# Kernel tuning notes

Hardware: AMD Instinct MI355X
Metric: run time of the kernel (lower is better)

## Reference

```python
import jax, jax.numpy as jnp
import numpy as np

B, S, BERT_H = 8, 512, 432
NL, HD = 12, 64
H = NL * HD  # 768
NEG = -1e12

def _lin(k, i, o):
    return jax.random.normal(k, (i, o), jnp.float32) * 0.02

def setup_inputs():
    key = jax.random.key(0)
    ks = jax.random.split(key, 12)
    return {
        "bert_hidden": jax.random.normal(ks[0], (B, S, BERT_H), jnp.float32),
        "attention_mask": jnp.ones((B, S), jnp.float32),
        "dense_w": _lin(ks[1], BERT_H, H), "dense_b": jnp.zeros((H,)),
        "sat_qw": _lin(ks[2], H, H), "sat_qb": jnp.zeros((H,)),
        "sat_kw": _lin(ks[3], H, H), "sat_kb": jnp.zeros((H,)),
        "sat_vw": _lin(ks[4], H, H), "sat_vb": jnp.zeros((H,)),
        "sat_ow": _lin(ks[5], H, H), "sat_ob": jnp.zeros((H,)),
        "rel_qw": _lin(ks[6], H, H), "rel_qb": jnp.zeros((H,)),
        "rel_kw": _lin(ks[7], H, H), "rel_kb": jnp.zeros((H,)),
        "rel_vw": _lin(ks[8], H, H), "rel_vb": jnp.zeros((H,)),
        "rel_ow": _lin(ks[9], H, H), "rel_ob": jnp.zeros((H,)),
        "lns_w": jnp.ones((H,)), "lns_b": jnp.zeros((H,)),
        "lnr_w": jnp.ones((H,)), "lnr_b": jnp.zeros((H,)),
        "head_w": _lin(ks[10], H, 2 * HD), "head_b": jnp.zeros((2 * HD,)),
        "tail_w": _lin(ks[11], 2 * HD, 2 * NL), "tail_b": jnp.zeros((2 * NL,)),
    }

def _layernorm(x, w, b, eps=1e-12):
    u = x.mean(-1, keepdims=True)
    s = ((x - u) ** 2).mean(-1, keepdims=True)
    return w * (x - u) / jnp.sqrt(s + eps) + b

def _mha(q_in, k_in, v_in, wq, bq, wk, bk, wv, bv, wo, bo):
    # q_in: [N, Lq, H]; k_in/v_in: [N, Lk, H]; dropout is identity (eval)
    N, Lq, _ = q_in.shape
    Lk = k_in.shape[1]
    qh = (q_in @ wq + bq).reshape(N, Lq, NL, HD)
    kh = (k_in @ wk + bk).reshape(N, Lk, NL, HD)
    vh = (v_in @ wv + bv).reshape(N, Lk, NL, HD)
    scores = jnp.einsum('nqhd,nkhd->nhqk', qh, kh) / np.float32(np.sqrt(HD))
    probs = jax.nn.softmax(scores, axis=-1)
    ctx = jnp.einsum('nhqk,nkhd->nqhd', probs, vh).reshape(N, Lq, NL * HD)
    return ctx @ wo + bo + q_in

def _shift_back(x):
    # faithful torch cycle_shift(forward=False): circular roll left by 1
    return jnp.roll(x, -1, axis=1)

def _shift_fwd(x):
    # faithful to the torch sequential in-place loop in cycle_shift(forward=True):
    # out[0] = x[-1]; out[1:] = x[0] (each copy reads the already-overwritten slot)
    b, s, h = x.shape
    return jnp.concatenate([x[:, -1:, :], jnp.broadcast_to(x[:, :1, :], (b, s - 1, h))], axis=1)

def reference(bert_hidden, attention_mask, dense_w, dense_b,
              sat_qw, sat_qb, sat_kw, sat_kb, sat_vw, sat_vb, sat_ow, sat_ob,
              rel_qw, rel_qb, rel_kw, rel_kb, rel_vw, rel_vb, rel_ow, rel_ob,
              lns_w, lns_b, lnr_w, lnr_b, head_w, head_b, tail_w, tail_b):
    hidden0 = bert_hidden @ dense_w + dense_b  # [B,S,H]
    cs = hidden0
    center = cs.mean(axis=1)  # [B,H], avg_pool2d over seq dim
    for _ in range(2):
        before = _shift_back(cs)
        after = _shift_fwd(cs)
        center_exp = jnp.broadcast_to(center[:, None, :], cs.shape)
        concats = jnp.stack([before, cs, after, hidden0, center_exp], axis=2)  # [B,S,5,H]
        concats = concats.reshape(B * S, 5, H)
        q = cs.reshape(B * S, 1, H)
        sat = _mha(q, concats, concats, sat_qw, sat_qb, sat_kw, sat_kb, sat_vw, sat_vb, sat_ow, sat_ob)
        cs = _layernorm(jax.nn.relu(sat), lns_w, lns_b).reshape(B, S, H)
        cc = jnp.concatenate([center[:, None, :], cs], axis=1)  # [B,S+1,H]
        rel = _mha(center[:, None, :], cc, cc, rel_qw, rel_qb, rel_kw, rel_kb, rel_vw, rel_vb, rel_ow, rel_ob)
        center = _layernorm(jax.nn.relu(rel), lnr_w, lnr_b)[:, 0, :]
    outputs = cs @ head_w + head_b  # [B,S,2*HD]
    qw, kw = outputs[..., ::2], outputs[..., 1::2]  # [B,S,HD]
    pos = jnp.arange(S, dtype=jnp.float32)
    inv = jnp.power(10000.0, -2.0 * jnp.arange(HD // 2, dtype=jnp.float32) / HD)
    ang = pos[:, None] * inv[None, :]  # [S,HD//2]
    pe = jnp.stack([jnp.sin(ang), jnp.cos(ang)], axis=-1).reshape(S, HD)
    cos_pos = jnp.repeat(pe[:, 1::2], 2, axis=-1)  # [S,HD]
    sin_pos = jnp.repeat(pe[:, ::2], 2, axis=-1)
    def rot(x):
        x2 = jnp.stack([-x[..., 1::2], x[..., ::2]], axis=-1).reshape(x.shape)
        return x * cos_pos + x2 * sin_pos
    qw, kw = rot(qw), rot(kw)
    logits = jnp.einsum('bmd,bnd->bmn', qw, kw) / np.float32(np.sqrt(HD))  # [B,S,S]
    bias = jnp.einsum('bnh->bhn', outputs @ tail_w + tail_b) / 2.0  # [B,2*NL,S]
    logits = logits[:, None, :, :] + bias[:, ::2, None, :] + bias[:, 1::2, :, None]  # [B,NL,S,S]
    m1 = attention_mask[:, None, :, None]
    logits = logits * m1 + NEG * (1.0 - m1)
    m2 = attention_mask[:, None, None, :]
    logits = logits * m2 + NEG * (1.0 - m2)
    tril = jnp.tril(jnp.ones((S, S), logits.dtype), k=-1)
    return logits - tril * 1e12
```

## Files before the change

### kernel.cpp

```cpp
#include <hip/hip_runtime.h>
#include <cstdint>
#include <cstddef>

#define HH 768
#define SS 512
#define NBATCH 8
#define NLH 12
#define HDIM 64
#define BSROWS 4096
static constexpr float NEGV = -1000000000000.0f;

typedef unsigned short ushort_t;
typedef __attribute__((ext_vector_type(4))) float fx4;
typedef __attribute__((ext_vector_type(8))) short sx8;

__device__ __forceinline__ ushort_t f2bf(float f) {
  uint32_t u = __float_as_uint(f);
  uint32_t r = (u + 0x7FFFu + ((u >> 16) & 1u)) >> 16;
  return (ushort_t)r;
}
__device__ __forceinline__ float bf2f(ushort_t h) {
  return __uint_as_float(((uint32_t)h) << 16);
}
__device__ __forceinline__ float2 ldbf2(const ushort_t* p) {
  uint32_t u = *(const uint32_t*)p;
  return make_float2(__uint_as_float(u << 16), __uint_as_float(u & 0xffff0000u));
}

__device__ __forceinline__ void async_copy16(void* lds, const void* g) {
  __builtin_amdgcn_global_load_lds(
      (const __attribute__((address_space(1))) void*)g,
      (__attribute__((address_space(3))) void*)lds, 16, 0, 0);
}

__device__ __forceinline__ void gemm_core(
    char* arena, int bid, int nwg, int nx,
    const ushort_t* __restrict__ A, int lda,
    const ushort_t* __restrict__ B, int ldb,
    const float* __restrict__ bias,
    const ushort_t* __restrict__ resb,
    ushort_t* __restrict__ Cb, int ldo,
    ushort_t* __restrict__ Cb2, int ldo2, int nsplit, int K,
    float* __restrict__ colmean)
{
  ushort_t* As = (ushort_t*)arena;
  ushort_t* Bs = (ushort_t*)(arena + 16384);
  const int tid = threadIdx.x;
  const int q = nwg >> 3;
  const int xcd = bid & 7, sidx = bid >> 3;
  const int swz = xcd * q + sidx;
  const int bm = (swz / nx) * 128;
  const int bn = (swz % nx) * 128;
  const int l = tid & 63;
  const int w = tid >> 6;
  const int wr = w >> 1, wc = w & 1;
  const int r8 = tid >> 3;
  const int sl = tid & 7;

  fx4 acc[4][4];
#pragma unroll
  for (int m = 0; m < 4; ++m)
#pragma unroll
    for (int n = 0; n < 4; ++n) acc[m][n] = (fx4)0.f;

  for (int k0 = 0; k0 < K; k0 += 64) {
#pragma unroll
    for (int i = 0; i < 4; ++i) {
      int row = i * 32 + r8;
      int srcs = sl ^ (row & 7);
      async_copy16((char*)As + i * 4096 + tid * 16,
                   A + (size_t)(bm + row) * lda + k0 + srcs * 8);
    }
#pragma unroll
    for (int i = 0; i < 4; ++i) {
      int row = i * 32 + r8;
      int srcs = sl ^ (row & 7);
      async_copy16((char*)Bs + i * 4096 + tid * 16,
                   B + (size_t)(bn + row) * ldb + k0 + srcs * 8);
    }
    __syncthreads();
#pragma unroll
    for (int kk = 0; kk < 2; ++kk) {
      sx8 av[4], bv[4];
      const int so = (l >> 4) + kk * 4;
#pragma unroll
      for (int m = 0; m < 4; ++m) {
        int r = wr * 64 + m * 16 + (l & 15);
        av[m] = *(const sx8*)((const char*)As + r * 128 + ((so ^ (r & 7)) * 16));
      }
#pragma unroll
      for (int n = 0; n < 4; ++n) {
        int r = wc * 64 + n * 16 + (l & 15);
        bv[n] = *(const sx8*)((const char*)Bs + r * 128 + ((so ^ (r & 7)) * 16));
      }
#pragma unroll
      for (int m = 0; m < 4; ++m)
#pragma unroll
        for (int n = 0; n < 4; ++n)
          acc[m][n] = __builtin_amdgcn_mfma_f32_16x16x32_bf16(av[m], bv[n], acc[m][n], 0, 0, 0);
    }
    __syncthreads();
  }

  const bool second = (bn >= nsplit);
  ushort_t* dst = second ? Cb2 : Cb;
  const int ld = second ? ldo2 : ldo;
  const int csub = second ? nsplit : 0;
  const int cr0 = bm + wr * 64 + (l >> 4) * 4;
  const int cc0 = bn + wc * 64 + (l & 15);
#pragma unroll
  for (int m = 0; m < 4; ++m) {
#pragma unroll
    for (int n = 0; n < 4; ++n) {
      int col = cc0 + n * 16;
      float bcol = bias[col];
#pragma unroll
      for (int j = 0; j < 4; ++j) {
        int row = cr0 + m * 16 + j;
        size_t off = (size_t)row * ld + (col - csub);
        float v = acc[m][n][j] + bcol;
        if (resb) v += bf2f(resb[off]);
        dst[off] = f2bf(v);
      }
    }
  }

  if (colmean) {
    float* scr = (float*)arena;
    const int cid = wr * 4 + (l >> 4);
#pragma unroll
    for (int n = 0; n < 4; ++n) {
      int colL = wc * 64 + n * 16 + (l & 15);
      float t = 16.0f * bias[bn + colL];
#pragma unroll
      for (int m = 0; m < 4; ++m)
#pragma unroll
        for (int j = 0; j < 4; ++j) t += acc[m][n][j];
      scr[cid * 128 + colL] = t;
    }
    __syncthreads();
    if (tid < 128) {
      float scol = 0.f;
#pragma unroll
      for (int c = 0; c < 8; ++c) scol += scr[c * 128 + tid];
      atomicAdd(&colmean[(bm >> 9) * HH + bn + tid], scol * (1.0f / 512.0f));
    }
  }
}

struct SmallJob { const float* W; const float* bias; const float* res; float* C; };
struct SmallJobs { SmallJob j[5]; };

__device__ __forceinline__ void skinny_core(
    char* arena, int colblk,
    const float* __restrict__ A, const float* __restrict__ W,
    const float* __restrict__ bias, const float* __restrict__ res, float* __restrict__ C)
{
  float* As = (float*)arena;
  float* part = (float*)(arena + 24576);
  const int tid = threadIdx.x;
#pragma unroll
  for (int i = 0; i < 6; ++i) {
    int idx = tid * 4 + i * 1024;
    *(float4*)&As[idx] = *(const float4*)(A + idx);
  }
  __syncthreads();
  const int c = tid & 31;
  const int col = (colblk << 5) + c;
  const int ks = tid >> 5;
  const float* Wp = W + (size_t)(ks * 96) * HH + col;
  float acc[8] = {};
#pragma unroll 8
  for (int k = 0; k < 96; ++k) {
    float wv = Wp[(size_t)k * HH];
    const float* ap = &As[ks * 96 + k];
#pragma unroll
    for (int m = 0; m < 8; ++m)
      acc[m] = fmaf(ap[m * HH], wv, acc[m]);
  }
#pragma unroll
  for (int m = 0; m < 8; ++m)
    part[ks * 256 + m * 32 + c] = acc[m];
  __syncthreads();
  const int m = tid >> 5;
  const int c2 = tid & 31;
  float s = 0.f;
#pragma unroll
  for (int k = 0; k < 8; ++k) s += part[k * 256 + m * 32 + c2];
  const int outcol = (colblk << 5) + c2;
  float v = s + bias[outcol];
  if (res) v += res[(size_t)m * HH + outcol];
  C[(size_t)m * HH + outcol] = v;
}

__global__ __launch_bounds__(256) void gemm_bf16(
    const ushort_t* __restrict__ A, int lda,
    const ushort_t* __restrict__ B, int ldb,
    const float* __restrict__ bias,
    const ushort_t* __restrict__ resb,
    ushort_t* __restrict__ Cb, int ldo,
    ushort_t* __restrict__ Cb2, int ldo2, int nsplit, int K, int nx,
    float* __restrict__ colmean)
{
  __shared__ char arena[32768];
  gemm_core(arena, blockIdx.x, gridDim.x, nx, A, lda, B, ldb, bias, resb,
            Cb, ldo, Cb2, ldo2, nsplit, K, colmean);
}

__global__ __launch_bounds__(256) void qkv_center(
    const ushort_t* __restrict__ A, const ushort_t* __restrict__ B,
    const float* __restrict__ bias, ushort_t* __restrict__ Cb,
    SmallJobs jobs, const float* __restrict__ center)
{
  __shared__ char arena[32768];
  if (blockIdx.x < 576) {
    gemm_core(arena, blockIdx.x, 576, 18, A, HH, B, HH, bias, nullptr,
              Cb, 2304, nullptr, 0, 1 << 30, HH, nullptr);
  } else {
    int vb = blockIdx.x - 576;
    SmallJob jb = jobs.j[vb / 24];
    skinny_core(arena, vb % 24, center, jb.W, jb.bias, jb.res, jb.C);
  }
}

__global__ __launch_bounds__(256) void gemm_skinny(
    const float* __restrict__ A, SmallJobs jobs)
{
  __shared__ char arena[32768];
  SmallJob jb = jobs.j[blockIdx.y];
  skinny_core(arena, blockIdx.x, A, jb.W, jb.bias, jb.res, jb.C);
}

struct SmallJobs2 { SmallJob j[2]; };
__global__ __launch_bounds__(256) void skinny_ln(
    const float* __restrict__ relo, const float* __restrict__ lw, const float* __restrict__ lb,
    SmallJobs2 jobs)
{
  __shared__ float As[8 * HH];
  __shared__ float part[8 * 8 * 32];
  const int tid = threadIdx.x;
  const SmallJob job = jobs.j[blockIdx.y];
#pragma unroll
  for (int i = 0; i < 6; ++i) {
    int idx = tid * 4 + i * 1024;
    *(float4*)&As[idx] = *(const float4*)(relo + idx);
  }
  __syncthreads();
  {
    const int row = tid >> 5, lc = tid & 31;
    float s = 0.f, sq = 0.f;
#pragma unroll
    for (int e = 0; e < 24; ++e) {
      float x = fmaxf(As[row * HH + lc * 24 + e], 0.f);
      s += x; sq += x * x;
    }
#pragma unroll
    for (int d = 1; d < 32; d <<= 1) { s += __shfl_xor(s, d); sq += __shfl_xor(sq, d); }
    float mean = s * (1.0f / HH);
    float var = sq * (1.0f / HH) - mean * mean;
    float rstd = rsqrtf(var + 1e-12f);
#pragma unroll
    for (int e = 0; e < 24; ++e) {
      int cc = lc * 24 + e;
      float x = fmaxf(As[row * HH + cc], 0.f);
      As[row * HH + cc] = lw[cc] * (x - mean) * rstd + lb[cc];
    }
  }
  __syncthreads();
  const int c = tid & 31;
  const int col = (blockIdx.x << 5) + c;
  const int ks = tid >> 5;
  const float* Wp = job.W + (size_t)(ks * 96) * HH + col;
  float acc[8] = {};
#pragma unroll 8
  for (int k = 0; k < 96; ++k) {
    float wv = Wp[(size_t)k * HH];
    const float* ap = &As[ks * 96 + k];
#pragma unroll
    for (int m = 0; m < 8; ++m)
      acc[m] = fmaf(ap[m * HH], wv, acc[m]);
  }
#pragma unroll
  for (int m = 0; m < 8; ++m)
    part[ks * 256 + m * 32 + c] = acc[m];
  __syncthreads();
  const int m = tid >> 5;
  const int c2 = tid & 31;
  float s2 = 0.f;
#pragma unroll
  for (int k = 0; k < 8; ++k) s2 += part[k * 256 + m * 32 + c2];
  const int outcol = (blockIdx.x << 5) + c2;
  job.C[(size_t)m * HH + outcol] = s2 + job.bias[outcol];
}

__global__ __launch_bounds__(256) void rel_attn(
    const float* __restrict__ Qr, const float* __restrict__ Krc, const ushort_t* __restrict__ Kr,
    const float* __restrict__ Vrc, const ushort_t* __restrict__ Vr, int ldkv,
    float* __restrict__ ctx)
{
  int b = blockIdx.x, h = blockIdx.y;
  __shared__ float qs[64];
  __shared__ float sc[513];
  __shared__ float part[4][64];
  __shared__ float redm[4], redsum[4];
  int t = threadIdx.x, lane = t & 63, wave = t >> 6;
  if (t < 64) qs[t] = Qr[b * HH + h * HDIM + t];
  __syncthreads();
  for (int j = t; j < 513; j += 256) {
    float acc = 0.f;
    if (j == 0) {
      const float* kp = Krc + b * HH + h * HDIM;
#pragma unroll
      for (int d = 0; d < HDIM; ++d) acc = fmaf(qs[d], kp[d], acc);
    } else {
      const sx8* kv = (const sx8*)(Kr + (size_t)(b * SS + j - 1) * ldkv + h * HDIM);
#pragma unroll
      for (int dq = 0; dq < 8; ++dq) {
        sx8 v = kv[dq];
#pragma unroll
        for (int e = 0; e < 8; ++e)
          acc = fmaf(qs[dq * 8 + e], bf2f((ushort_t)v[e]), acc);
      }
    }
    sc[j] = acc * 0.125f;
  }
  __syncthreads();
  float m = -1e30f;
  for (int j = t; j < 513; j += 256) m = fmaxf(m, sc[j]);
#pragma unroll
  for (int d = 1; d < 64; d <<= 1) m = fmaxf(m, __shfl_xor(m, d));
  if (lane == 0) redm[wave] = m;
  __syncthreads();
  m = fmaxf(fmaxf(redm[0], redm[1]), fmaxf(redm[2], redm[3]));
  float lsum = 0.f;
  for (int j = t; j < 513; j += 256) { float e = __expf(sc[j] - m); sc[j] = e; lsum += e; }
#pragma unroll
  for (int d = 1; d < 64; d <<= 1) lsum += __shfl_xor(lsum, d);
  if (lane == 0) redsum[wave] = lsum;
  __syncthreads();
  float total = redsum[0] + redsum[1] + redsum[2] + redsum[3];
  float accv = 0.f;
#pragma unroll 8
  for (int j = wave; j < 513; j += 4) {
    float vv = (j == 0) ? Vrc[b * HH + h * HDIM + lane]
                        : bf2f(Vr[(size_t)(b * SS + j - 1) * ldkv + h * HDIM + lane]);
    accv = fmaf(sc[j], vv, accv);
  }
  part[wave][lane] = accv;
  __syncthreads();
  if (wave == 0) {
    float r = (part[0][lane] + part[1][lane] + part[2][lane] + part[3][lane]) / total;
    ctx[b * HH + h * HDIM + lane] = r;
  }
}

__global__ __launch_bounds__(256) void head_fused(
    const ushort_t* __restrict__ Araw,
    const float* __restrict__ lnw, const float* __restrict__ lnb,
    const ushort_t* __restrict__ B,
    const float* __restrict__ head_b,
    const float* __restrict__ tail_w,
    const float* __restrict__ tail_b,
    float* __restrict__ qw, float* __restrict__ kw,
    float* __restrict__ bias2)
{
  __shared__ ushort_t As[16 * 64];
  __shared__ ushort_t Bs[128 * 64];
  __shared__ float tile[16][130];
  __shared__ float invt[32];
  __shared__ float2 rst[16];
  const int tid = threadIdx.x;
  const int bm = blockIdx.x * 16;
  const int l = tid & 63;
  const int w = tid >> 6;
  const int r8 = tid >> 3;
  const int sl = tid & 7;

  if (tid < 32) invt[tid] = powf(10000.0f, -(float)tid / 32.0f);

  {
    int row = tid >> 4, part = tid & 15;
    const ushort_t* rp = Araw + (size_t)(bm + row) * HH + part * 48;
    float s = 0.f, sq = 0.f;
#pragma unroll
    for (int c = 0; c < 6; ++c) {
      sx8 v = *(const sx8*)(rp + c * 8);
#pragma unroll
      for (int e = 0; e < 8; ++e) {
        float x = fmaxf(bf2f((ushort_t)v[e]), 0.f);
        s += x; sq += x * x;
      }
    }
#pragma unroll
    for (int d = 1; d < 16; d <<= 1) { s += __shfl_xor(s, d); sq += __shfl_xor(sq, d); }
    if (part == 0) {
      float mean = s * (1.0f / HH);
      float var = sq * (1.0f / HH) - mean * mean;
      rst[row] = make_float2(mean, rsqrtf(var + 1e-12f));
    }
  }
  __syncthreads();

  fx4 acc[2];
  acc[0] = (fx4)0.f; acc[1] = (fx4)0.f;

  for (int k0 = 0; k0 < HH; k0 += 64) {
#pragma unroll
    for (int i = 0; i < 4; ++i) {
      int row = i * 32 + r8;
      int srcs = sl ^ (row & 7);
      async_copy16((char*)Bs + i * 4096 + tid * 16,
                   B + (size_t)row * HH + k0 + srcs * 8);
    }
    if (tid < 128) {
      int row = tid >> 3;
      int slot = sl ^ (row & 7);
      int gk = k0 + slot * 8;
      sx8 v = *(const sx8*)(Araw + (size_t)(bm + row) * HH + gk);
      float4 w0 = *(const float4*)(lnw + gk);
      float4 w1 = *(const float4*)(lnw + gk + 4);
      float4 b0 = *(const float4*)(lnb + gk);
      float4 b1 = *(const float4*)(lnb + gk + 4);
      float wv[8] = {w0.x, w0.y, w0.z, w0.w, w1.x, w1.y, w1.z, w1.w};
      float bv[8] = {b0.x, b0.y, b0.z, b0.w, b1.x, b1.y, b1.z, b1.w};
      float2 mr = rst[row];
      sx8 ov;
#pragma unroll
      for (int e = 0; e < 8; ++e) {
        float x = fmaxf(bf2f((ushort_t)v[e]), 0.f);
        ov[e] = (short)f2bf(fmaf((x - mr.x) * mr.y, wv[e], bv[e]));
      }
      *(sx8*)((char*)As + row * 128 + sl * 16) = ov;
    }
    __syncthreads();
#pragma unroll
    for (int kk = 0; kk < 2; ++kk) {
      const int so = (l >> 4) + kk * 4;
      int ra = l & 15;
      sx8 av = *(const sx8*)((const char*)As + ra * 128 + ((so ^ (ra & 7)) * 16));
#pragma unroll
      for (int n = 0; n < 2; ++n) {
        int r = w * 32 + n * 16 + (l & 15);
        sx8 bv = *(const sx8*)((const char*)Bs + r * 128 + ((so ^ (r & 7)) * 16));
        acc[n] = __builtin_amdgcn_mfma_f32_16x16x32_bf16(av, bv, acc[n], 0, 0, 0);
      }
    }
    __syncthreads();
  }

  {
    const int rr0 = (l >> 4) * 4;
#pragma unroll
    for (int n = 0; n < 2; ++n) {
      int col = w * 32 + n * 16 + (l & 15);
      float bcol = head_b[col];
#pragma unroll
      for (int j = 0; j < 4; ++j)
        tile[rr0 + j][col] = acc[n][j] + bcol;
    }
  }
  __syncthreads();

#pragma unroll
  for (int it = 0; it < 2; ++it) {
    int t = tid + it * 256;
    int r = t >> 5, i = t & 31;
    int s = (bm + r) & 511;
    float ang = (float)s * invt[i];
    float sn = sinf(ang), cn = cosf(ang);
    float q0 = tile[r][4 * i + 0], k0 = tile[r][4 * i + 1];
    float q1 = tile[r][4 * i + 2], k1 = tile[r][4 * i + 3];
    float* qp = qw + (size_t)(bm + r) * 64 + i * 2;
    float* kp = kw + (size_t)(bm + r) * 64 + i * 2;
    qp[0] = q0 * cn - q1 * sn; qp[1] = q1 * cn + q0 * sn;
    kp[0] = k0 * cn - k1 * sn; kp[1] = k1 * cn + k0 * sn;
  }
  for (int t = tid; t < 16 * 24; t += 256) {
    int r = t / 24, c = t % 24;
    float acc2 = tail_b[c];
#pragma unroll 16
    for (int k = 0; k < 128; ++k) acc2 = fmaf(tile[r][k], tail_w[k * 24 + c], acc2);
    bias2[(size_t)(bm + r) * 24 + c] = acc2 * 0.5f;
  }
}

struct TJob { const float* src; ushort_t* dst; int K, N, Kpad, rowOff; };
struct PrepArgs {
  TJob j[8];
  const float* bert; ushort_t* bert_bf;
  const float* rkb; const float* rvb; const float* sqb; const float* skb; const float* svb;
  float* b_merged;
  float* center;
};
__global__ __launch_bounds__(256) void prep_all(PrepArgs pa)
{
  if (blockIdx.z < 8) {
    TJob jb = pa.j[blockIdx.z];
    int k0 = blockIdx.x * 32, n0 = blockIdx.y * 32;
    if (k0 >= jb.Kpad || n0 >= jb.N) return;
    __shared__ float t[32][33];
    int tx = threadIdx.x & 31, ty = threadIdx.x >> 5;
#pragma unroll
    for (int i = 0; i < 4; ++i) {
      int k = k0 + ty + i * 8;
      float v = 0.f;
      if (k < jb.K && n0 + tx < jb.N) v = jb.src[(size_t)k * jb.N + n0 + tx];
      t[ty + i * 8][tx] = v;
    }
    __syncthreads();
#pragma unroll
    for (int i = 0; i < 4; ++i) {
      int n = n0 + ty + i * 8;
      int k = k0 + tx;
      if (n < jb.N && k < jb.Kpad)
        jb.dst[(size_t)(jb.rowOff + n) * jb.Kpad + k] = f2bf(t[tx][ty + i * 8]);
    }
  } else {
    const int NB = BSROWS * 448;
    const int total = NB + 3840 + NBATCH * HH;
    int start = (blockIdx.y * 24 + blockIdx.x) * 256 + threadIdx.x;
    for (int i = start; i < total; i += 24 * 24 * 256) {
      if (i < NB) {
        int r = i / 448, c = i % 448;
        pa.bert_bf[i] = (c < 432) ? f2bf(pa.bert[(size_t)r * 432 + c]) : (ushort_t)0;
      } else if (i < NB + 3840) {
        int c = i - NB;
        float v;
        if (c < 768) v = pa.rkb[c];
        else if (c < 1536) v = pa.rvb[c - 768];
        else if (c < 2304) v = pa.sqb[c - 1536];
        else if (c < 3072) v = pa.skb[c - 2304];
        else v = pa.svb[c - 3072];
        pa.b_merged[c] = v;
      } else {
        pa.center[i - NB - 3840] = 0.f;
      }
    }
  }
}

__global__ __launch_bounds__(256) void sat_attn(
    const ushort_t* __restrict__ Qc, const ushort_t* __restrict__ Kc,
    const ushort_t* __restrict__ Vc, int ldq,
    const ushort_t* __restrict__ Kh0, const ushort_t* __restrict__ Vh0, int ldh,
    const float* __restrict__ Kcen, const float* __restrict__ Vcen,
    ushort_t* __restrict__ ctxb)
{
  int i = blockIdx.x;
  int b = i >> 9, s = i & 511;
  int lane = threadIdx.x & 63;
  int wave = threadIdx.x >> 6;
  size_t rb = (size_t)(b * SS + ((s + 1) & 511));
  size_t rs = (size_t)i;
  size_t ra = (size_t)(b * SS + (s == 0 ? (SS - 1) : 0));
  size_t rc = (size_t)b * HH;
  const int half = lane >> 5;
  const int d0 = (lane & 31) * 2;
#pragma unroll
  for (int it = 0; it < 2; ++it) {
    int p = wave + 4 * it;
    if (p >= 6) break;
    int off = (2 * p + half) * HDIM + d0;
    float2 q  = ldbf2(Qc + rs * ldq + off);
    float2 kb = ldbf2(Kc + rb * ldq + off);
    float2 ks = ldbf2(Kc + rs * ldq + off);
    float2 ka = ldbf2(Kc + ra * ldq + off);
    float2 kh = ldbf2(Kh0 + rs * ldh + off);
    float2 kc = *(const float2*)(Kcen + rc + off);
    float s0 = q.x * kb.x + q.y * kb.y;
    float s1 = q.x * ks.x + q.y * ks.y;
    float s2 = q.x * ka.x + q.y * ka.y;
    float s3 = q.x * kh.x + q.y * kh.y;
    float s4 = q.x * kc.x + q.y * kc.y;
#pragma unroll
    for (int d = 1; d < 32; d <<= 1) {
      s0 += __shfl_xor(s0, d); s1 += __shfl_xor(s1, d); s2 += __shfl_xor(s2, d);
      s3 += __shfl_xor(s3, d); s4 += __shfl_xor(s4, d);
    }
    const float sc = 0.125f;
    s0 *= sc; s1 *= sc; s2 *= sc; s3 *= sc; s4 *= sc;
    float mx = fmaxf(fmaxf(fmaxf(s0, s1), fmaxf(s2, s3)), s4);
    float e0 = __expf(s0 - mx), e1 = __expf(s1 - mx), e2 = __expf(s2 - mx);
    float e3 = __expf(s3 - mx), e4 = __expf(s4 - mx);
    float inv = 1.f / (e0 + e1 + e2 + e3 + e4);
    float2 vb = ldbf2(Vc + rb * ldq + off);
    float2 vs = ldbf2(Vc + rs * ldq + off);
    float2 va = ldbf2(Vc + ra * ldq + off);
    float2 vh = ldbf2(Vh0 + rs * ldh + off);
    float2 vc = *(const float2*)(Vcen + rc + off);
    float vx = e0 * vb.x + e1 * vs.x + e2 * va.x + e3 * vh.x + e4 * vc.x;
    float vy = e0 * vb.y + e1 * vs.y + e2 * va.y + e3 * vh.y + e4 * vc.y;
    uint32_t o = (uint32_t)f2bf(vx * inv) | ((uint32_t)f2bf(vy * inv) << 16);
    *(uint32_t*)(ctxb + rs * HH + off) = o;
  }
}

__global__ __launch_bounds__(256) void relu_ln_bf(
    const ushort_t* __restrict__ x, const float* __restrict__ w, const float* __restrict__ b,
    ushort_t* __restrict__ ybf)
{
  int row = blockIdx.x;
  const ushort_t* xr = x + (size_t)row * HH;
  float v[3];
  float sum = 0.f, sumsq = 0.f;
#pragma unroll
  for (int j = 0; j < 3; ++j) {
    float t = bf2f(xr[threadIdx.x + j * 256]);
    t = fmaxf(t, 0.f);
    v[j] = t;
    sum += t; sumsq += t * t;
  }
#pragma unroll
  for (int d = 1; d < 64; d <<= 1) { sum += __shfl_xor(sum, d); sumsq += __shfl_xor(sumsq, d); }
  __shared__ float ws_[4], wsq_[4];
  int wave = threadIdx.x >> 6, lane = threadIdx.x & 63;
  if (lane == 0) { ws_[wave] = sum; wsq_[wave] = sumsq; }
  __syncthreads();
  sum = ws_[0] + ws_[1] + ws_[2] + ws_[3];
  sumsq = wsq_[0] + wsq_[1] + wsq_[2] + wsq_[3];
  float mean = sum * (1.0f / HH);
  float var = sumsq * (1.0f / HH) - mean * mean;
  float rstd = rsqrtf(var + 1e-12f);
#pragma unroll
  for (int j = 0; j < 3; ++j) {
    int cidx = threadIdx.x + j * 256;
    float o = w[cidx] * (v[j] - mean) * rstd + b[cidx];
    ybf[(size_t)row * HH + cidx] = f2bf(o);
  }
}

__global__ __launch_bounds__(256) void final_kernel(
    const float* __restrict__ qw, const float* __restrict__ kw,
    const float* __restrict__ bias2, const float* __restrict__ mask,
    float* __restrict__ out)
{
  int b = blockIdx.z;
  int mt = blockIdx.y * 32;
  int nt = blockIdx.x * 32;
  __shared__ float qs[32][68];
  __shared__ float ks[32][68];
  int t = threadIdx.x;
  {
    int idx = t * 8;
    int r = idx >> 6, c = idx & 63;
    const float* sq = qw + (size_t)(b * SS + mt + r) * 64 + c;
    const float* sk = kw + (size_t)(b * SS + nt + r) * 64 + c;
    *(float4*)&qs[r][c]     = *(const float4*)(sq);
    *(float4*)&qs[r][c + 4] = *(const float4*)(sq + 4);
    *(float4*)&ks[r][c]     = *(const float4*)(sk);
    *(float4*)&ks[r][c + 4] = *(const float4*)(sk + 4);
  }
  __syncthreads();
  int m = t >> 3;
  int n0 = (t & 7) * 4;
  float d0 = 0.f, d1 = 0.f, d2 = 0.f, d3 = 0.f;
#pragma unroll
  for (int d = 0; d < 64; d += 4) {
    float4 qv = *(const float4*)&qs[m][d];
    float4 k0 = *(const float4*)&ks[n0 + 0][d];
    float4 k1 = *(const float4*)&ks[n0 + 1][d];
    float4 k2 = *(const float4*)&ks[n0 + 2][d];
    float4 k3 = *(const float4*)&ks[n0 + 3][d];
    d0 += qv.x * k0.x + qv.y * k0.y + qv.z * k0.z + qv.w * k0.w;
    d1 += qv.x * k1.x + qv.y * k1.y + qv.z * k1.z + qv.w * k1.w;
    d2 += qv.x * k2.x + qv.y * k2.y + qv.z * k2.z + qv.w * k2.w;
    d3 += qv.x * k3.x + qv.y * k3.y + qv.z * k3.z + qv.w * k3.w;
  }
  int gm = mt + m;
  int gn = nt + n0;
  d0 *= 0.125f; d1 *= 0.125f; d2 *= 0.125f; d3 *= 0.125f;
  float mm = mask[b * SS + gm];
  float mn0 = mask[b * SS + gn + 0];
  float mn1 = mask[b * SS + gn + 1];
  float mn2 = mask[b * SS + gn + 2];
  float mn3 = mask[b * SS + gn + 3];
  const float* bmp  = bias2 + (size_t)(b * SS + gm) * 24;
  const float* bnp0 = bias2 + (size_t)(b * SS + gn + 0) * 24;
  const float* bnp1 = bias2 + (size_t)(b * SS + gn + 1) * 24;
  const float* bnp2 = bias2 + (size_t)(b * SS + gn + 2) * 24;
  const float* bnp3 = bias2 + (size_t)(b * SS + gn + 3) * 24;
#pragma unroll
  for (int h = 0; h < NLH; ++h) {
    float tb = bmp[2 * h + 1];
    float v0 = d0 + bnp0[2 * h] + tb;
    float v1 = d1 + bnp1[2 * h] + tb;
    float v2 = d2 + bnp2[2 * h] + tb;
    float v3 = d3 + bnp3[2 * h] + tb;
    v0 = v0 * mm + NEGV * (1.f - mm); v1 = v1 * mm + NEGV * (1.f - mm);
    v2 = v2 * mm + NEGV * (1.f - mm); v3 = v3 * mm + NEGV * (1.f - mm);
    v0 = v0 * mn0 + NEGV * (1.f - mn0); v1 = v1 * mn1 + NEGV * (1.f - mn1);
    v2 = v2 * mn2 + NEGV * (1.f - mn2); v3 = v3 * mn3 + NEGV * (1.f - mn3);
    if (gm > gn + 0) v0 -= 1000000000000.0f;
    if (gm > gn + 1) v1 -= 1000000000000.0f;
    if (gm > gn + 2) v2 -= 1000000000000.0f;
    if (gm > gn + 3) v3 -= 1000000000000.0f;
    float4 o = make_float4(v0, v1, v2, v3);
    *(float4*)(out + ((((size_t)(b * NLH + h)) * SS + gm) * SS + gn)) = o;
  }
}

extern "C" void kernel_launch(void* const* d_in, const int* in_sizes, int n_in,
                              void* d_out, int out_size, void* d_ws, size_t ws_size,
                              hipStream_t stream)
{
  const float* bert    = (const float*)d_in[0];
  const float* amask   = (const float*)d_in[1];
  const float* dense_w = (const float*)d_in[2];
  const float* dense_b = (const float*)d_in[3];
  const float* sat_qw  = (const float*)d_in[4];
  const float* sat_qb  = (const float*)d_in[5];
  const float* sat_kw  = (const float*)d_in[6];
  const float* sat_kb  = (const float*)d_in[7];
  const float* sat_vw  = (const float*)d_in[8];
  const float* sat_vb  = (const float*)d_in[9];
  const float* sat_ow  = (const float*)d_in[10];
  const float* sat_ob  = (const float*)d_in[11];
  const float* rel_qw  = (const float*)d_in[12];
  const float* rel_qb  = (const float*)d_in[13];
  const float* rel_kw  = (const float*)d_in[14];
  const float* rel_kb  = (const float*)d_in[15];
  const float* rel_vw  = (const float*)d_in[16];
  const float* rel_vb  = (const float*)d_in[17];
  const float* rel_ow  = (const float*)d_in[18];
  const float* rel_ob  = (const float*)d_in[19];
  const float* lns_w   = (const float*)d_in[20];
  const float* lns_b   = (const float*)d_in[21];
  const float* lnr_w   = (const float*)d_in[22];
  const float* lnr_b   = (const float*)d_in[23];
  const float* head_w  = (const float*)d_in[24];
  const float* head_b  = (const float*)d_in[25];
  const float* tail_w  = (const float*)d_in[26];
  const float* tail_b  = (const float*)d_in[27];

  float* out = (float*)d_out;
  char*  ws  = (char*)d_ws;

  size_t off = 0;
  auto alloc = [&](size_t bytes) { char* p = ws + off; off += (bytes + 255) & ~(size_t)255; return p; };
  ushort_t* bert_bf   = (ushort_t*)alloc((size_t)BSROWS * 448 * 2);
  ushort_t* Wt_dense  = (ushort_t*)alloc((size_t)768 * 448 * 2);
  ushort_t* Wt_big    = (ushort_t*)alloc((size_t)3840 * 768 * 2);
  ushort_t* Wt_satow  = (ushort_t*)alloc((size_t)768 * 768 * 2);
  ushort_t* Wt_head   = (ushort_t*)alloc((size_t)128 * 768 * 2);
  ushort_t* hidden0_bf= (ushort_t*)alloc((size_t)BSROWS * HH * 2);
  ushort_t* ctx_bf    = (ushort_t*)alloc((size_t)BSROWS * HH * 2);
  ushort_t* csA_bf    = (ushort_t*)alloc((size_t)BSROWS * HH * 2);
  float* b_merged = (float*)alloc(3840 * 4);
  float* center   = (float*)alloc(6144 * 4);
  float* Kcen     = (float*)alloc(6144 * 4);
  float* Vcen     = (float*)alloc(6144 * 4);
  float* Qr       = (float*)alloc(6144 * 4);
  float* Krc      = (float*)alloc(6144 * 4);
  float* Vrc      = (float*)alloc(6144 * 4);
  float* ctxr     = (float*)alloc(6144 * 4);
  float* relo     = (float*)alloc(6144 * 4);
  float* bias2    = (float*)alloc((size_t)BSROWS * 24 * 4);
  float* qwbuf    = (float*)alloc((size_t)BSROWS * 64 * 4);
  float* kwbuf    = (float*)alloc((size_t)BSROWS * 64 * 4);

  ushort_t* QKV1_bf = (ushort_t*)out;
  ushort_t* tmp1_bf = QKV1_bf + (size_t)BSROWS * 2304;
  ushort_t* KrVr_bf = tmp1_bf + (size_t)BSROWS * 768;
  ushort_t* QKV2_bf = KrVr_bf + (size_t)BSROWS * 1536;
  ushort_t* tmp2_bf = tmp1_bf;

  dim3 blk(256);

  {
    PrepArgs pa;
    pa.j[0] = { dense_w, Wt_dense, 432, 768, 448, 0 };
    pa.j[1] = { rel_kw,  Wt_big,   768, 768, 768, 0 };
    pa.j[2] = { rel_vw,  Wt_big,   768, 768, 768, 768 };
    pa.j[3] = { sat_qw,  Wt_big,   768, 768, 768, 1536 };
    pa.j[4] = { sat_kw,  Wt_big,   768, 768, 768, 2304 };
    pa.j[5] = { sat_vw,  Wt_big,   768, 768, 768, 3072 };
    pa.j[6] = { sat_ow,  Wt_satow, 768, 768, 768, 0 };
    pa.j[7] = { head_w,  Wt_head,  768, 128, 768, 0 };
    pa.bert = bert; pa.bert_bf = bert_bf;
    pa.rkb = rel_kb; pa.rvb = rel_vb; pa.sqb = sat_qb; pa.skb = sat_kb; pa.svb = sat_vb;
    pa.b_merged = b_merged; pa.center = center;
    prep_all<<<dim3(24, 24, 9), blk, 0, stream>>>(pa);
  }

  gemm_bf16<<<dim3(192), blk, 0, stream>>>(bert_bf, 448, Wt_dense, 448, dense_b,
                                           nullptr, hidden0_bf, HH,
                                           nullptr, 0, 1 << 30, 448, 6, center);

  {
    SmallJobs jobs;
    jobs.j[0] = { sat_kw, sat_kb, nullptr, Kcen };
    jobs.j[1] = { sat_vw, sat_vb, nullptr, Vcen };
    jobs.j[2] = { rel_qw, rel_qb, nullptr, Qr };
    jobs.j[3] = { rel_kw, rel_kb, nullptr, Krc };
    jobs.j[4] = { rel_vw, rel_vb, nullptr, Vrc };
    qkv_center<<<dim3(696), blk, 0, stream>>>(hidden0_bf, Wt_big + (size_t)1536 * 768,
                                              b_merged + 1536, QKV1_bf, jobs, center);
  }
  sat_attn<<<BSROWS, 256, 0, stream>>>(QKV1_bf, QKV1_bf + 768, QKV1_bf + 1536, 2304,
                                       QKV1_bf + 768, QKV1_bf + 1536, 2304,
                                       Kcen, Vcen, ctx_bf);
  gemm_bf16<<<dim3(192), blk, 0, stream>>>(ctx_bf, HH, Wt_satow, HH, sat_ob,
                                           hidden0_bf, tmp1_bf, HH,
                                           nullptr, 0, 1 << 30, HH, 6, nullptr);
  relu_ln_bf<<<BSROWS, 256, 0, stream>>>(tmp1_bf, lns_w, lns_b, csA_bf);

  gemm_bf16<<<dim3(960), blk, 0, stream>>>(csA_bf, HH, Wt_big, HH, b_merged,
                                           nullptr, KrVr_bf, 1536,
                                           QKV2_bf, 2304, 1536, HH, 30, nullptr);
  rel_attn<<<dim3(8, 12), 256, 0, stream>>>(Qr, Krc, KrVr_bf, Vrc, KrVr_bf + 768, 1536, ctxr);
  {
    SmallJobs jobs;
    jobs.j[0] = { rel_ow, rel_ob, center, relo };
    gemm_skinny<<<dim3(24, 1), blk, 0, stream>>>(ctxr, jobs);
  }
  {
    SmallJobs2 jobs;
    jobs.j[0] = { sat_kw, sat_kb, nullptr, Kcen };
    jobs.j[1] = { sat_vw, sat_vb, nullptr, Vcen };
    skinny_ln<<<dim3(24, 2), blk, 0, stream>>>(relo, lnr_w, lnr_b, jobs);
  }
  sat_attn<<<BSROWS, 256, 0, stream>>>(QKV2_bf, QKV2_bf + 768, QKV2_bf + 1536, 2304,
                                       QKV1_bf + 768, QKV1_bf + 1536, 2304,
                                       Kcen, Vcen, ctx_bf);
  gemm_bf16<<<dim3(192), blk, 0, stream>>>(ctx_bf, HH, Wt_satow, HH, sat_ob,
                                           csA_bf, tmp2_bf, HH,
                                           nullptr, 0, 1 << 30, HH, 6, nullptr);
  head_fused<<<256, blk, 0, stream>>>(tmp2_bf, lns_w, lns_b, Wt_head, head_b,
                                      tail_w, tail_b, qwbuf, kwbuf, bias2);
  final_kernel<<<dim3(16, 16, 8), 256, 0, stream>>>(qwbuf, kwbuf, bias2, amask, out);
}
```

Before: 266.0 us.

## Fuse relation attention and output projection into the second QKV GEMM launch

Splits the combined Kr/Vr + QKV2 GEMM into two launches: one computes Kr/Vr, and a second runs the sat QKV2 GEMM tiles alongside per-(batch, head) relation-attention blocks. Those blocks also apply the rel_ow projection through atomicAdd into a buffer zeroed in prep, so the separate rel_attn and skinny GEMM kernels are removed. The bias and residual add moves into skinny_ln. The sat_attn block index is also permuted to interleave batches. The aim is fewer launches and overlapping the small attention work with GEMM tiles, at the cost of atomic contention and float summation order that is no longer deterministic.

Result: faster. 256.8 us, median of 3 (-3.5%).

```diff
diff --git a/kernel.cpp b/kernel.cpp
--- a/kernel.cpp
+++ b/kernel.cpp
@@ -193,6 +193,81 @@
   C[(size_t)m * HH + outcol] = v;
 }
 
+__device__ __forceinline__ void rel_core(
+    char* arena, int b, int h,
+    const float* __restrict__ Qr, const float* __restrict__ Krc, const ushort_t* __restrict__ Kr,
+    const float* __restrict__ Vrc, const ushort_t* __restrict__ Vr,
+    const float* __restrict__ rel_ow, float* __restrict__ relo)
+{
+  float* qs = (float*)arena;
+  float* sc = (float*)(arena + 256);
+  float* part = (float*)(arena + 2560);
+  float* redm = (float*)(arena + 3584);
+  float* redsum = (float*)(arena + 3600);
+  float* ctxs = (float*)(arena + 3616);
+  int t = threadIdx.x, lane = t & 63, wave = t >> 6;
+  if (t < 64) qs[t] = Qr[b * HH + h * HDIM + t];
+  __syncthreads();
+  for (int j = t; j < 513; j += 256) {
+    float acc = 0.f;
+    if (j == 0) {
+      const float* kp = Krc + b * HH + h * HDIM;
+#pragma unroll
+      for (int d = 0; d < HDIM; ++d) acc = fmaf(qs[d], kp[d], acc);
+    } else {
+      const sx8* kv = (const sx8*)(Kr + (size_t)(b * SS + j - 1) * 1536 + h * HDIM);
+#pragma unroll
+      for (int dq = 0; dq < 8; ++dq) {
+        sx8 v = kv[dq];
+#pragma unroll
+        for (int e = 0; e < 8; ++e)
+          acc = fmaf(qs[dq * 8 + e], bf2f((ushort_t)v[e]), acc);
+      }
+    }
+    sc[j] = acc * 0.125f;
+  }
+  __syncthreads();
+  float m = -1e30f;
+  for (int j = t; j < 513; j += 256) m = fmaxf(m, sc[j]);
+#pragma unroll
+  for (int d = 1; d < 64; d <<= 1) m = fmaxf(m, __shfl_xor(m, d));
+  if (lane == 0) redm[wave] = m;
+  __syncthreads();
+  m = fmaxf(fmaxf(redm[0], redm[1]), fmaxf(redm[2], redm[3]));
+  float lsum = 0.f;
+  for (int j = t; j < 513; j += 256) { float e = __expf(sc[j] - m); sc[j] = e; lsum += e; }
+#pragma unroll
+  for (int d = 1; d < 64; d <<= 1) lsum += __shfl_xor(lsum, d);
+  if (lane == 0) redsum[wave] = lsum;
+  __syncthreads();
+  float total = redsum[0] + redsum[1] + redsum[2] + redsum[3];
+  float accv = 0.f;
+#pragma unroll 8
+  for (int j = wave; j < 513; j += 4) {
+    float vv = (j == 0) ? Vrc[b * HH + h * HDIM + lane]
+                        : bf2f(Vr[(size_t)(b * SS + j - 1) * 1536 + h * HDIM + lane]);
+    accv = fmaf(sc[j], vv, accv);
+  }
+  part[wave * 64 + lane] = accv;
+  __syncthreads();
+  if (wave == 0)
+    ctxs[lane] = (part[0 * 64 + lane] + part[1 * 64 + lane] +
+                  part[2 * 64 + lane] + part[3 * 64 + lane]) / total;
+  __syncthreads();
+  for (int c = t; c < HH; c += 256) {
+    const float* Wp = rel_ow + (size_t)(h * 64) * HH + c;
+    float a0 = 0.f, a1 = 0.f, a2 = 0.f, a3 = 0.f;
+#pragma unroll
+    for (int d = 0; d < 64; d += 4) {
+      a0 = fmaf(ctxs[d + 0], Wp[(size_t)(d + 0) * HH], a0);
+      a1 = fmaf(ctxs[d + 1], Wp[(size_t)(d + 1) * HH], a1);
+      a2 = fmaf(ctxs[d + 2], Wp[(size_t)(d + 2) * HH], a2);
+      a3 = fmaf(ctxs[d + 3], Wp[(size_t)(d + 3) * HH], a3);
+    }
+    atomicAdd(&relo[b * HH + c], (a0 + a1) + (a2 + a3));
+  }
+}
+
 __global__ __launch_bounds__(256) void gemm_bf16(
     const ushort_t* __restrict__ A, int lda,
     const ushort_t* __restrict__ B, int ldb,
@@ -223,17 +298,29 @@
   }
 }
 
-__global__ __launch_bounds__(256) void gemm_skinny(
-    const float* __restrict__ A, SmallJobs jobs)
+__global__ __launch_bounds__(256) void qkv2_rel(
+    const ushort_t* __restrict__ A, const ushort_t* __restrict__ B,
+    const float* __restrict__ bias, ushort_t* __restrict__ Cb,
+    const float* __restrict__ Qr, const float* __restrict__ Krc,
+    const ushort_t* __restrict__ Kr,
+    const float* __restrict__ Vrc, const ushort_t* __restrict__ Vr,
+    const float* __restrict__ rel_ow, float* __restrict__ relo)
 {
   __shared__ char arena[32768];
-  SmallJob jb = jobs.j[blockIdx.y];
-  skinny_core(arena, blockIdx.x, A, jb.W, jb.bias, jb.res, jb.C);
+  if (blockIdx.x < 576) {
+    gemm_core(arena, blockIdx.x, 576, 18, A, HH, B, HH, bias, nullptr,
+              Cb, 2304, nullptr, 0, 1 << 30, HH, nullptr);
+  } else {
+    int v = blockIdx.x - 576;
+    rel_core(arena, v / 12, v % 12, Qr, Krc, Kr, Vrc, Vr, rel_ow, relo);
+  }
 }
 
 struct SmallJobs2 { SmallJob j[2]; };
 __global__ __launch_bounds__(256) void skinny_ln(
-    const float* __restrict__ relo, const float* __restrict__ lw, const float* __restrict__ lb,
+    const float* __restrict__ relo, const float* __restrict__ rel_ob,
+    const float* __restrict__ center,
+    const float* __restrict__ lw, const float* __restrict__ lb,
     SmallJobs2 jobs)
 {
   __shared__ float As[8 * HH];
@@ -243,7 +330,15 @@
 #pragma unroll
   for (int i = 0; i < 6; ++i) {
     int idx = tid * 4 + i * 1024;
-    *(float4*)&As[idx] = *(const float4*)(relo + idx);
+    int row = idx / HH;
+    int col = idx - row * HH;
+    float4 r4 = *(const float4*)(relo + idx);
+    float4 o4 = *(const float4*)(rel_ob + col);
+    float4 c4 = *(const float4*)(center + idx);
+    As[idx + 0] = r4.x + o4.x + c4.x;
+    As[idx + 1] = r4.y + o4.y + c4.y;
+    As[idx + 2] = r4.z + o4.z + c4.z;
+    As[idx + 3] = r4.w + o4.w + c4.w;
   }
   __syncthreads();
   {
@@ -291,67 +386,6 @@
   for (int k = 0; k < 8; ++k) s2 += part[k * 256 + m * 32 + c2];
   const int outcol = (blockIdx.x << 5) + c2;
   job.C[(size_t)m * HH + outcol] = s2 + job.bias[outcol];
-}
-
-__global__ __launch_bounds__(256) void rel_attn(
-    const float* __restrict__ Qr, const float* __restrict__ Krc, const ushort_t* __restrict__ Kr,
-    const float* __restrict__ Vrc, const ushort_t* __restrict__ Vr, int ldkv,
-    float* __restrict__ ctx)
-{
-  int b = blockIdx.x, h = blockIdx.y;
-  __shared__ float qs[64];
-  __shared__ float sc[513];
-  __shared__ float part[4][64];
-  __shared__ float redm[4], redsum[4];
-  int t = threadIdx.x, lane = t & 63, wave = t >> 6;
-  if (t < 64) qs[t] = Qr[b * HH + h * HDIM + t];
-  __syncthreads();
-  for (int j = t; j < 513; j += 256) {
-    float acc = 0.f;
-    if (j == 0) {
-      const float* kp = Krc + b * HH + h * HDIM;
-#pragma unroll
-      for (int d = 0; d < HDIM; ++d) acc = fmaf(qs[d], kp[d], acc);
-    } else {
-      const sx8* kv = (const sx8*)(Kr + (size_t)(b * SS + j - 1) * ldkv + h * HDIM);
-#pragma unroll
-      for (int dq = 0; dq < 8; ++dq) {
-        sx8 v = kv[dq];
-#pragma unroll
-        for (int e = 0; e < 8; ++e)
-          acc = fmaf(qs[dq * 8 + e], bf2f((ushort_t)v[e]), acc);
-      }
-    }
-    sc[j] = acc * 0.125f;
-  }
-  __syncthreads();
-  float m = -1e30f;
-  for (int j = t; j < 513; j += 256) m = fmaxf(m, sc[j]);
-#pragma unroll
-  for (int d = 1; d < 64; d <<= 1) m = fmaxf(m, __shfl_xor(m, d));
-  if (lane == 0) redm[wave] = m;
-  __syncthreads();
-  m = fmaxf(fmaxf(redm[0], redm[1]), fmaxf(redm[2], redm[3]));
-  float lsum = 0.f;
-  for (int j = t; j < 513; j += 256) { float e = __expf(sc[j] - m); sc[j] = e; lsum += e; }
-#pragma unroll
-  for (int d = 1; d < 64; d <<= 1) lsum += __shfl_xor(lsum, d);
-  if (lane == 0) redsum[wave] = lsum;
-  __syncthreads();
-  float total = redsum[0] + redsum[1] + redsum[2] + redsum[3];
-  float accv = 0.f;
-#pragma unroll 8
-  for (int j = wave; j < 513; j += 4) {
-    float vv = (j == 0) ? Vrc[b * HH + h * HDIM + lane]
-                        : bf2f(Vr[(size_t)(b * SS + j - 1) * ldkv + h * HDIM + lane]);
-    accv = fmaf(sc[j], vv, accv);
-  }
-  part[wave][lane] = accv;
-  __syncthreads();
-  if (wave == 0) {
-    float r = (part[0][lane] + part[1][lane] + part[2][lane] + part[3][lane]) / total;
-    ctx[b * HH + h * HDIM + lane] = r;
-  }
 }
 
 __global__ __launch_bounds__(256) void head_fused(
@@ -491,6 +525,7 @@
   const float* rkb; const float* rvb; const float* sqb; const float* skb; const float* svb;
   float* b_merged;
   float* center;
+  float* relo;
 };
 __global__ __launch_bounds__(256) void prep_all(PrepArgs pa)
 {
@@ -517,7 +552,7 @@
     }
   } else {
     const int NB = BSROWS * 448;
-    const int total = NB + 3840 + NBATCH * HH;
+    const int total = NB + 3840 + 2 * NBATCH * HH;
     int start = (blockIdx.y * 24 + blockIdx.x) * 256 + threadIdx.x;
     for (int i = start; i < total; i += 24 * 24 * 256) {
       if (i < NB) {
@@ -532,8 +567,10 @@
         else if (c < 3072) v = pa.skb[c - 2304];
         else v = pa.svb[c - 3072];
         pa.b_merged[c] = v;
+      } else if (i < NB + 3840 + NBATCH * HH) {
+        pa.center[i - NB - 3840] = 0.f;
       } else {
-        pa.center[i - NB - 3840] = 0.f;
+        pa.relo[i - NB - 3840 - NBATCH * HH] = 0.f;
       }
     }
   }
@@ -546,7 +583,7 @@
     const float* __restrict__ Kcen, const float* __restrict__ Vcen,
     ushort_t* __restrict__ ctxb)
 {
-  int i = blockIdx.x;
+  int i = ((blockIdx.x & 7) << 9) | (blockIdx.x >> 3);
   int b = i >> 9, s = i & 511;
   int lane = threadIdx.x & 63;
   int wave = threadIdx.x >> 6;
@@ -752,7 +789,6 @@
   float* Qr       = (float*)alloc(6144 * 4);
   float* Krc      = (float*)alloc(6144 * 4);
   float* Vrc      = (float*)alloc(6144 * 4);
-  float* ctxr     = (float*)alloc(6144 * 4);
   float* relo     = (float*)alloc(6144 * 4);
   float* bias2    = (float*)alloc((size_t)BSROWS * 24 * 4);
   float* qwbuf    = (float*)alloc((size_t)BSROWS * 64 * 4);
@@ -778,7 +814,7 @@
     pa.j[7] = { head_w,  Wt_head,  768, 128, 768, 0 };
     pa.bert = bert; pa.bert_bf = bert_bf;
     pa.rkb = rel_kb; pa.rvb = rel_vb; pa.sqb = sat_qb; pa.skb = sat_kb; pa.svb = sat_vb;
-    pa.b_merged = b_merged; pa.center = center;
+    pa.b_merged = b_merged; pa.center = center; pa.relo = relo;
     prep_all<<<dim3(24, 24, 9), blk, 0, stream>>>(pa);
   }
 
@@ -804,20 +840,18 @@
                                            nullptr, 0, 1 << 30, HH, 6, nullptr);
   relu_ln_bf<<<BSROWS, 256, 0, stream>>>(tmp1_bf, lns_w, lns_b, csA_bf);
 
-  gemm_bf16<<<dim3(960), blk, 0, stream>>>(csA_bf, HH, Wt_big, HH, b_merged,
+  gemm_bf16<<<dim3(480), blk, 0, stream>>>(csA_bf, HH, Wt_big, HH, b_merged,
                                            nullptr, KrVr_bf, 1536,
-                                           QKV2_bf, 2304, 1536, HH, 30, nullptr);
-  rel_attn<<<dim3(8, 12), 256, 0, stream>>>(Qr, Krc, KrVr_bf, Vrc, KrVr_bf + 768, 1536, ctxr);
-  {
-    SmallJobs jobs;
-    jobs.j[0] = { rel_ow, rel_ob, center, relo };
-    gemm_skinny<<<dim3(24, 1), blk, 0, stream>>>(ctxr, jobs);
-  }
+                                           nullptr, 0, 1 << 30, HH, 12, nullptr);
+  qkv2_rel<<<dim3(672), blk, 0, stream>>>(csA_bf, Wt_big + (size_t)1536 * 768,
+                                          b_merged + 1536, QKV2_bf,
+                                          Qr, Krc, KrVr_bf, Vrc, KrVr_bf + 768,
+                                          rel_ow, relo);
   {
     SmallJobs2 jobs;
     jobs.j[0] = { sat_kw, sat_kb, nullptr, Kcen };
     jobs.j[1] = { sat_vw, sat_vb, nullptr, Vcen };
-    skinny_ln<<<dim3(24, 2), blk, 0, stream>>>(relo, lnr_w, lnr_b, jobs);
+    skinny_ln<<<dim3(24, 2), blk, 0, stream>>>(relo, rel_ob, center, lnr_w, lnr_b, jobs);
   }
   sat_attn<<<BSROWS, 256, 0, stream>>>(QKV2_bf, QKV2_bf + 768, QKV2_bf + 1536, 2304,
                                        QKV1_bf + 768, QKV1_bf + 1536, 2304,
```
